# Performance work log

Hardware: AMD Instinct MI355X
Metric: run time of the kernel (lower is better)

Reference implementation:

```python
import jax, jax.numpy as jnp
import numpy as np

B, N_P, N_S = 64, 50, 200
N_NODES = N_P * N_S          # 10000 nodes per graph (jobs x ops)
N_CAND = N_S + 1             # 201 candidates
INPUT_DIM, HIDDEN = 3, 64
NODE_DIM = 2 * HIDDEN        # h_nodes feature dim (=> actor in = 6*HIDDEN)
POOL_DIM = 4 * HIDDEN        # h_pooled dim (mean || max pooling)
H_ACTOR, H_CRITIC = 256, 256


def setup_inputs() -> dict:
    key = jax.random.key(0)
    ks = jax.random.split(key, 16)
    p = lambda k, sh: jax.random.normal(k, sh, jnp.float32) * 0.02
    x = jax.random.normal(ks[0], (B, N_NODES, INPUT_DIM), jnp.float32)
    candidate = jax.random.randint(ks[1], (B, N_CAND), 0, N_NODES)
    mask = jax.random.randint(ks[2], (B, N_CAND), 0, 2) > 0
    mask = mask.at[:, 0].set(True)  # guarantee at least one valid action per row
    return {
        "x": x, "candidate": candidate, "mask": mask,
        "fe_w1": p(ks[3], (INPUT_DIM, HIDDEN)), "fe_b1": jnp.zeros((HIDDEN,), jnp.float32),
        "fe_w2": p(ks[4], (HIDDEN, NODE_DIM)), "fe_b2": jnp.zeros((NODE_DIM,), jnp.float32),
        "a_w1": p(ks[5], (NODE_DIM + POOL_DIM, H_ACTOR)), "a_b1": jnp.zeros((H_ACTOR,), jnp.float32),
        "a_w2": p(ks[6], (H_ACTOR, H_ACTOR)), "a_b2": jnp.zeros((H_ACTOR,), jnp.float32),
        "a_w3": p(ks[7], (H_ACTOR, 1)), "a_b3": jnp.zeros((1,), jnp.float32),
        "c_w1": p(ks[8], (POOL_DIM, H_CRITIC)), "c_b1": jnp.zeros((H_CRITIC,), jnp.float32),
        "c_w2": p(ks[9], (H_CRITIC, H_CRITIC)), "c_b2": jnp.zeros((H_CRITIC,), jnp.float32),
        "c_w3": p(ks[10], (H_CRITIC, 1)), "c_b3": jnp.zeros((1,), jnp.float32),
    }


def _actor_critic(x, candidate, mask,
                  fe_w1, fe_b1, fe_w2, fe_b2,
                  a_w1, a_b1, a_w2, a_b2, a_w3, a_b3,
                  c_w1, c_b1, c_w2, c_b2, c_w3, c_b3):
    # --- feature_extract: per-node MLP embedding, graph-level pooling ---
    h = jax.nn.relu(jnp.einsum('bni,ih->bnh', x, fe_w1) + fe_b1)
    h_nodes = jax.nn.relu(jnp.einsum('bnh,hd->bnd', h, fe_w2) + fe_b2)   # [B, N, 2H]
    h_pooled = jnp.concatenate([h_nodes.mean(axis=1), h_nodes.max(axis=1)], axis=-1)  # [B, 4H]

    # --- gather candidate node features (torch.gather over node axis) ---
    cand_feat = jnp.take_along_axis(h_nodes, candidate[:, :, None], axis=1)  # [B, C, 2H]

    # --- concat broadcast pooled feature ---
    pooled_rep = jnp.broadcast_to(h_pooled[:, None, :], (cand_feat.shape[0], cand_feat.shape[1], h_pooled.shape[-1]))
    concat_fea = jnp.concatenate([cand_feat, pooled_rep], axis=-1)  # [B, C, 6H]

    # --- actor MLP (tanh hidden layers, linear out) ---
    a = jnp.tanh(concat_fea @ a_w1 + a_b1)
    a = jnp.tanh(a @ a_w2 + a_b2)
    scores = a @ a_w3 + a_b3                                    # [B, C, 1]

    # --- mask with -inf, softmax over candidate axis ---
    scores = jnp.where(mask[:, :, None], scores, -jnp.inf)
    pi = jax.nn.softmax(scores, axis=1)                          # [B, C, 1]

    # --- critic MLP on pooled feature ---
    c = jnp.tanh(h_pooled @ c_w1 + c_b1)
    c = jnp.tanh(c @ c_w2 + c_b2)
    v = c @ c_w3 + c_b3                                          # [B, 1]
    return pi, v


def reference(x, candidate, mask,
              fe_w1, fe_b1, fe_w2, fe_b2,
              a_w1, a_b1, a_w2, a_b2, a_w3, a_b3,
              c_w1, c_b1, c_w2, c_b2, c_w3, c_b3):
    return _actor_critic(x, candidate, mask,
                         fe_w1, fe_b1, fe_w2, fe_b2,
                         a_w1, a_b1, a_w2, a_b2, a_w3, a_b3,
                         c_w1, c_b1, c_w2, c_b2, c_w3, c_b3)
```

## Files before the change

### kernel.cpp

```cpp
#include <hip/hip_runtime.h>

#define NN 10000
#define NCAND 201
#define NB 64

typedef __attribute__((ext_vector_type(8))) short short8;
typedef __attribute__((ext_vector_type(4))) float f32x4;

__device__ __forceinline__ float bf2f(unsigned short u) {
  return __uint_as_float(((unsigned int)u) << 16);
}
__device__ __forceinline__ unsigned short f2bf(float f) {
  unsigned int u = __float_as_uint(f);
  u += 0x7FFFu + ((u >> 16) & 1u);
  return (unsigned short)(u >> 16);
}
__device__ __forceinline__ float fast_tanh(float x) {
  return 1.0f - 2.0f / (__expf(2.0f * x) + 1.0f);
}
__device__ __forceinline__ float gld(const void* p, long i, int f) {
  return f ? ((const float*)p)[i] : bf2f(((const unsigned short*)p)[i]);
}

__global__ __launch_bounds__(256)
void detect_kernel(const void* x, const void* w1, const void* b1, const void* w2,
                   const void* b2, const void* aw1, const void* ab1, const void* aw2,
                   const void* ab2, const void* aw3, const void* ab3,
                   const void* cw1, const void* cb1, const void* cw2, const void* cb2,
                   const void* cw3, const void* cb3,
                   const unsigned int* mask_w, const unsigned int* cand_w,
                   int* F) {
  const void* ptrs[17] = {x, w1, b1, w2, b2, aw1, ab1, aw2, ab2, aw3, ab3,
                          cw1, cb1, cw2, cb2, cw3, cb3};
  const int sizes[17] = {1920000, 192, 64, 8192, 128, 98304, 256, 65536, 256,
                         256, 1, 65536, 256, 65536, 256, 256, 1};
  const int t = threadIdx.x;
  const int j = blockIdx.x;
  __shared__ int sh[3];
  if (t < 3) sh[t] = 0;
  __syncthreads();
  if (j < 17) {
    const unsigned short* p = (const unsigned short*)ptrs[j];
    int K = min(sizes[j], 2048);
    int c = 0;
    for (int i = t; i < K; i += 256)
      if ((p[i] & 0x7F80u) >= 0x4300u) c++;
    if (c) atomicAdd(&sh[0], c);
    __syncthreads();
    if (t == 0) F[j] = (sh[0] > (K >> 3)) ? 1 : 0;
  } else if (j == 17) {
    int flo = 0, fhi = 0, fgt = 0;
    for (int i = t; i < 3216; i += 256) {
      unsigned int w = mask_w[i];
      if ((w & 0xFFFFu) == 0x3F80u) flo = 1;
      if ((w >> 16) == 0x3F80u) fhi = 1;
      if (w > 1u) fgt = 1;
    }
    if (flo) sh[0] = 1;
    if (fhi) sh[1] = 1;
    if (fgt) sh[2] = 1;
    __syncthreads();
    if (t == 0) F[17] = sh[0] ? 2 : (sh[1] ? 3 : (sh[2] ? 1 : 0));
  } else {
    int co = 0;
    for (int i = t; i < 1024; i += 256)
      if ((i & 1) && cand_w[i] != 0u) co = 1;
    if (co) sh[0] = 1;
    __syncthreads();
    if (t == 0) F[18] = sh[0] ? 0 : 1;
  }
}

__global__ __launch_bounds__(256)
void prep_kernel(const void* __restrict__ fe_w2, const void* __restrict__ a_w1,
                 const void* __restrict__ a_w2,
                 const void* __restrict__ c_w1, const void* __restrict__ c_w2,
                 const int* __restrict__ F,
                 unsigned short* __restrict__ w2t, unsigned short* __restrict__ aw1t,
                 unsigned short* __restrict__ aw2t,
                 unsigned short* __restrict__ cw1t, unsigned short* __restrict__ cw2t) {
  const int F3 = F[3], F5 = F[5], F7 = F[7], F11 = F[11], F13 = F[13];
  int i = blockIdx.x * 256 + threadIdx.x;
  if (i < 128 * 64) { int n = i >> 6, k = i & 63; w2t[i] = f2bf(gld(fe_w2, k * 128 + n, F3)); }
  if (i < 256 * 384) { int n = i / 384, k = i % 384; aw1t[i] = f2bf(gld(a_w1, k * 256 + n, F5)); }
  if (i < 256 * 256) {
    int n = i >> 8, k = i & 255;
    aw2t[i] = f2bf(gld(a_w2, k * 256 + n, F7));
    cw1t[i] = f2bf(gld(c_w1, k * 256 + n, F11));
    cw2t[i] = f2bf(gld(c_w2, k * 256 + n, F13));
  }
}

__global__ __launch_bounds__(256, 4)
void feat_pool_kernel(const void* __restrict__ x,
                      const void* __restrict__ w1, const void* __restrict__ b1,
                      const unsigned short* __restrict__ w2t,
                      const void* __restrict__ b2,
                      const int* __restrict__ F,
                      float* __restrict__ psum, float* __restrict__ pmax) {
  __shared__ __align__(16) unsigned short h1s[64 * 72];
  __shared__ float w1f[3 * 64];
  __shared__ float b1f[64];
  __shared__ float b2f[128];

  const int t = threadIdx.x;
  const int b = blockIdx.x >> 5;
  const int s = blockIdx.x & 31;
  const int lane = t & 63;
  const int wv = t >> 6;
  const int F0 = F[0], F1 = F[1], F2 = F[2], F4 = F[4];

  if (t < 192) w1f[t] = gld(w1, t, F1);
  if (t < 64) b1f[t] = gld(b1, t, F2);
  if (t < 128) b2f[t] = gld(b2, t, F4);

  short8 bfr[2][2];
#pragma unroll
  for (int nl = 0; nl < 2; ++nl)
#pragma unroll
    for (int ks = 0; ks < 2; ++ks) {
      int col = wv * 32 + nl * 16 + (lane & 15);
      bfr[nl][ks] = *(const short8*)(w2t + col * 64 + ((lane >> 4) * 8) + ks * 32);
    }
  __syncthreads();

  float csum[2] = {0.f, 0.f};
  float cmax[2] = {0.f, 0.f};

  for (int c = s; c < 157; c += 32) {
    int nb = c * 64;
    int cnt = (nb + 64 <= NN) ? 64 : (NN - nb);
    {
      int m = t & 63;
      if (m < cnt) {
        long xo = ((long)b * NN + nb + m) * 3;
        float x0 = gld(x, xo, F0), x1 = gld(x, xo + 1, F0), x2 = gld(x, xo + 2, F0);
        int kg = t >> 6;
        short8 v0, v1;
#pragma unroll
        for (int i = 0; i < 8; ++i) {
          int k = kg * 16 + i;
          float v = x0 * w1f[k] + x1 * w1f[64 + k] + x2 * w1f[128 + k] + b1f[k];
          v0[i] = (short)f2bf(fmaxf(v, 0.f));
        }
#pragma unroll
        for (int i = 0; i < 8; ++i) {
          int k = kg * 16 + 8 + i;
          float v = x0 * w1f[k] + x1 * w1f[64 + k] + x2 * w1f[128 + k] + b1f[k];
          v1[i] = (short)f2bf(fmaxf(v, 0.f));
        }
        *(short8*)(h1s + m * 72 + kg * 16) = v0;
        *(short8*)(h1s + m * 72 + kg * 16 + 8) = v1;
      }
    }
    __syncthreads();
#pragma unroll
    for (int mt = 0; mt < 4; ++mt) {
      const unsigned short* ap = h1s + (mt * 16 + (lane & 15)) * 72 + ((lane >> 4) * 8);
      short8 af0 = *(const short8*)(ap);
      short8 af1 = *(const short8*)(ap + 32);
#pragma unroll
      for (int nl = 0; nl < 2; ++nl) {
        f32x4 acc = {0.f, 0.f, 0.f, 0.f};
        acc = __builtin_amdgcn_mfma_f32_16x16x32_bf16(af0, bfr[nl][0], acc, 0, 0, 0);
        acc = __builtin_amdgcn_mfma_f32_16x16x32_bf16(af1, bfr[nl][1], acc, 0, 0, 0);
        int col = wv * 32 + nl * 16 + (lane & 15);
        float bb = b2f[col];
#pragma unroll
        for (int r = 0; r < 4; ++r) {
          int row = mt * 16 + ((lane >> 4) * 4) + r;
          if (row < cnt) {
            float v = fmaxf(acc[r] + bb, 0.f);
            csum[nl] += v;
            cmax[nl] = fmaxf(cmax[nl], v);
          }
        }
      }
    }
    __syncthreads();
  }
#pragma unroll
  for (int nl = 0; nl < 2; ++nl) {
    csum[nl] += __shfl_xor(csum[nl], 16);
    csum[nl] += __shfl_xor(csum[nl], 32);
    cmax[nl] = fmaxf(cmax[nl], __shfl_xor(cmax[nl], 16));
    cmax[nl] = fmaxf(cmax[nl], __shfl_xor(cmax[nl], 32));
  }
  if (lane < 16) {
#pragma unroll
    for (int nl = 0; nl < 2; ++nl) {
      int col = wv * 32 + nl * 16 + lane;
      atomicAdd(&psum[b * 128 + col], csum[nl]);
      atomicMax((int*)&pmax[b * 128 + col], __float_as_int(cmax[nl]));
    }
  }
}

__global__ __launch_bounds__(256)
void actor_kernel(const void* __restrict__ x, const int* __restrict__ cand,
                  const void* __restrict__ w1, const void* __restrict__ b1,
                  const void* __restrict__ b2bf,
                  const void* __restrict__ ab1, const void* __restrict__ ab2,
                  const void* __restrict__ aw3, const void* __restrict__ ab3,
                  const int* __restrict__ F,
                  const float* __restrict__ psum, const float* __restrict__ pmax,
                  const unsigned short* __restrict__ w2t,
                  const unsigned short* __restrict__ aw1t,
                  const unsigned short* __restrict__ aw2t,
                  float* __restrict__ scores) {
  __shared__ __align__(16) unsigned short h1c[32 * 72];
  __shared__ __align__(16) unsigned short cf[32 * 136];
  __shared__ __align__(16) unsigned short a1s[32 * 264];
  __shared__ __align__(16) unsigned short a2s[32 * 264];
  __shared__ __align__(16) unsigned short plbf[256];
  __shared__ float ab1f[256], ab2f[256], b2f[128];

  const int t = threadIdx.x;
  const int b = blockIdx.x / 7;
  const int cb = blockIdx.x % 7;
  const int cbase = cb * 29;
  const int cntc = min(29, NCAND - cbase);
  const int lane = t & 63;
  const int wv = t >> 6;
  const int F0 = F[0], F1 = F[1], F2 = F[2], F4 = F[4], F6 = F[6], F8 = F[8];
  const int F9 = F[9], F10 = F[10], C64 = F[18];

  if (t < 128) {
    plbf[t] = f2bf(psum[b * 128 + t] * (1.0f / 10000.0f));
    plbf[128 + t] = f2bf(pmax[b * 128 + t]);
    b2f[t] = gld(b2bf, t, F4);
  }
  ab1f[t] = gld(ab1, t, F6);
  ab2f[t] = gld(ab2, t, F8);

  {
    int r = t & 31;
    int ci = cbase + r;
    if (ci > NCAND - 1) ci = NCAND - 1;
    long cidx = (long)b * NCAND + ci;
    int nd = C64 ? cand[2 * cidx] : cand[cidx];
    long xo = ((long)b * NN + nd) * 3;
    float x0 = gld(x, xo, F0), x1 = gld(x, xo + 1, F0), x2 = gld(x, xo + 2, F0);
    int kg = t >> 5;
#pragma unroll
    for (int i = 0; i < 8; ++i) {
      int k = kg * 8 + i;
      float v = x0 * gld(w1, k, F1) + x1 * gld(w1, 64 + k, F1) +
                x2 * gld(w1, 128 + k, F1) + gld(b1, k, F2);
      h1c[r * 72 + k] = f2bf(fmaxf(v, 0.f));
    }
  }
  __syncthreads();

  {
    short8 af[2][2];
#pragma unroll
    for (int mt = 0; mt < 2; ++mt)
#pragma unroll
      for (int ks = 0; ks < 2; ++ks)
        af[mt][ks] = *(const short8*)(h1c + (mt * 16 + (lane & 15)) * 72 + ((lane >> 4) * 8) + ks * 32);
#pragma unroll
    for (int nl = 0; nl < 2; ++nl) {
      int col = wv * 32 + nl * 16 + (lane & 15);
      short8 bf0 = *(const short8*)(w2t + col * 64 + ((lane >> 4) * 8));
      short8 bf1 = *(const short8*)(w2t + col * 64 + ((lane >> 4) * 8) + 32);
      float bb = b2f[col];
#pragma unroll
      for (int mt = 0; mt < 2; ++mt) {
        f32x4 acc = {0.f, 0.f, 0.f, 0.f};
        acc = __builtin_amdgcn_mfma_f32_16x16x32_bf16(af[mt][0], bf0, acc, 0, 0, 0);
        acc = __builtin_amdgcn_mfma_f32_16x16x32_bf16(af[mt][1], bf1, acc, 0, 0, 0);
#pragma unroll
        for (int r = 0; r < 4; ++r) {
          int row = mt * 16 + ((lane >> 4) * 4) + r;
          cf[row * 136 + col] = f2bf(fmaxf(acc[r] + bb, 0.f));
        }
      }
    }
  }
  __syncthreads();

  {
    f32x4 acc[2][4];
#pragma unroll
    for (int mt = 0; mt < 2; ++mt)
#pragma unroll
      for (int nt = 0; nt < 4; ++nt) acc[mt][nt] = (f32x4){0.f, 0.f, 0.f, 0.f};
    for (int ks = 0; ks < 12; ++ks) {
      short8 af0, af1;
      if (ks < 4) {
        af0 = *(const short8*)(cf + (lane & 15) * 136 + ks * 32 + ((lane >> 4) * 8));
        af1 = *(const short8*)(cf + (16 + (lane & 15)) * 136 + ks * 32 + ((lane >> 4) * 8));
      } else {
        short8 p = *(const short8*)(plbf + (ks - 4) * 32 + ((lane >> 4) * 8));
        af0 = p;
        af1 = p;
      }
#pragma unroll
      for (int nt = 0; nt < 4; ++nt) {
        int col = wv * 64 + nt * 16 + (lane & 15);
        short8 bfr = *(const short8*)(aw1t + col * 384 + ks * 32 + ((lane >> 4) * 8));
        acc[0][nt] = __builtin_amdgcn_mfma_f32_16x16x32_bf16(af0, bfr, acc[0][nt], 0, 0, 0);
        acc[1][nt] = __builtin_amdgcn_mfma_f32_16x16x32_bf16(af1, bfr, acc[1][nt], 0, 0, 0);
      }
    }
#pragma unroll
    for (int mt = 0; mt < 2; ++mt)
#pragma unroll
      for (int nt = 0; nt < 4; ++nt) {
        int col = wv * 64 + nt * 16 + (lane & 15);
        float bb = ab1f[col];
#pragma unroll
        for (int r = 0; r < 4; ++r) {
          int row = mt * 16 + ((lane >> 4) * 4) + r;
          a1s[row * 264 + col] = f2bf(fast_tanh(acc[mt][nt][r] + bb));
        }
      }
  }
  __syncthreads();

  {
    f32x4 acc[2][4];
#pragma unroll
    for (int mt = 0; mt < 2; ++mt)
#pragma unroll
      for (int nt = 0; nt < 4; ++nt) acc[mt][nt] = (f32x4){0.f, 0.f, 0.f, 0.f};
    for (int ks = 0; ks < 8; ++ks) {
      short8 af0 = *(const short8*)(a1s + (lane & 15) * 264 + ks * 32 + ((lane >> 4) * 8));
      short8 af1 = *(const short8*)(a1s + (16 + (lane & 15)) * 264 + ks * 32 + ((lane >> 4) * 8));
#pragma unroll
      for (int nt = 0; nt < 4; ++nt) {
        int col = wv * 64 + nt * 16 + (lane & 15);
        short8 bfr = *(const short8*)(aw2t + col * 256 + ks * 32 + ((lane >> 4) * 8));
        acc[0][nt] = __builtin_amdgcn_mfma_f32_16x16x32_bf16(af0, bfr, acc[0][nt], 0, 0, 0);
        acc[1][nt] = __builtin_amdgcn_mfma_f32_16x16x32_bf16(af1, bfr, acc[1][nt], 0, 0, 0);
      }
    }
#pragma unroll
    for (int mt = 0; mt < 2; ++mt)
#pragma unroll
      for (int nt = 0; nt < 4; ++nt) {
        int col = wv * 64 + nt * 16 + (lane & 15);
        float bb = ab2f[col];
#pragma unroll
        for (int r = 0; r < 4; ++r) {
          int row = mt * 16 + ((lane >> 4) * 4) + r;
          a2s[row * 264 + col] = f2bf(fast_tanh(acc[mt][nt][r] + bb));
        }
      }
  }
  __syncthreads();

  {
    int row = t >> 3, seg = t & 7;
    float p = 0.f;
#pragma unroll 8
    for (int i = 0; i < 32; ++i) {
      int k = seg * 32 + i;
      p += bf2f(a2s[row * 264 + k]) * gld(aw3, k, F9);
    }
    p += __shfl_xor(p, 1);
    p += __shfl_xor(p, 2);
    p += __shfl_xor(p, 4);
    if (seg == 0 && row < cntc)
      scores[b * 256 + cbase + row] = p + gld(ab3, 0, F10);
  }
}

__global__ __launch_bounds__(256)
void softmax_critic_kernel(const float* __restrict__ scores,
                           const void* __restrict__ mask,
                           const int* __restrict__ F,
                           const float* __restrict__ psum,
                           const float* __restrict__ pmax,
                           const unsigned short* __restrict__ cw1t,
                           const unsigned short* __restrict__ cw2t,
                           const void* __restrict__ cb1, const void* __restrict__ cb2,
                           const void* __restrict__ cw3, const void* __restrict__ cb3,
                           void* __restrict__ out) {
  __shared__ float plf[256];
  __shared__ float c1f[256];
  __shared__ float red[4];
  const int t = threadIdx.x, b = blockIdx.x;
  const int lane = t & 63, wv = t >> 6;
  const int MM = F[17];
  const int OF = (F[0] + F[1] + F[3] + F[5] + F[7] + F[9] + F[11] + F[13] + F[15]) >= 5;
  const int F12 = F[12], F14 = F[14], F15 = F[15], F16 = F[16];

  if (t < 128) {
    plf[t] = psum[b * 128 + t] * (1.0f / 10000.0f);
    plf[128 + t] = pmax[b * 128 + t];
  }

  float sraw = 0.f, sv = -1e30f;
  bool valid = false;
  if (t < NCAND) {
    sraw = scores[b * 256 + t];
    long idx = (long)b * NCAND + t;
    if (MM == 0)      valid = ((const int*)mask)[idx] != 0;
    else if (MM == 1) valid = ((const unsigned char*)mask)[idx] != 0;
    else if (MM == 2) valid = ((const unsigned short*)mask)[idx] != 0;
    else              valid = ((const unsigned int*)mask)[idx] != 0;
    if (valid) sv = sraw;
  }
  float m = sv;
  for (int o = 32; o; o >>= 1) m = fmaxf(m, __shfl_xor(m, o));
  if (lane == 0) red[wv] = m;
  __syncthreads();
  m = fmaxf(fmaxf(red[0], red[1]), fmaxf(red[2], red[3]));
  __syncthreads();
  float e = valid ? __expf(sraw - m) : 0.f;
  if (!(e == e)) e = 0.f;
  float ss = e;
  for (int o = 32; o; o >>= 1) ss += __shfl_xor(ss, o);
  if (lane == 0) red[wv] = ss;
  __syncthreads();
  float tot = red[0] + red[1] + red[2] + red[3];
  tot = fmaxf(tot, 1e-30f);
  if (t < NCAND) {
    float pv = e / tot;
    if (!(pv == pv)) pv = 0.f;
    if (OF) ((float*)out)[b * NCAND + t] = pv;
    else ((unsigned short*)out)[b * NCAND + t] = f2bf(pv);
  }
  __syncthreads();

  {
    float a = gld(cb1, t, F12);
    const unsigned short* row = cw1t + t * 256;
#pragma unroll
    for (int k8 = 0; k8 < 32; ++k8) {
      short8 w = *(const short8*)(row + k8 * 8);
#pragma unroll
      for (int j = 0; j < 8; ++j)
        a += plf[k8 * 8 + j] * bf2f((unsigned short)w[j]);
    }
    c1f[t] = fast_tanh(a);
  }
  __syncthreads();
  {
    float a2 = gld(cb2, t, F14);
    const unsigned short* row = cw2t + t * 256;
#pragma unroll
    for (int k8 = 0; k8 < 32; ++k8) {
      short8 w = *(const short8*)(row + k8 * 8);
#pragma unroll
      for (int j = 0; j < 8; ++j)
        a2 += c1f[k8 * 8 + j] * bf2f((unsigned short)w[j]);
    }
    a2 = fast_tanh(a2);
    float p = a2 * gld(cw3, t, F15);
    for (int o = 32; o; o >>= 1) p += __shfl_xor(p, o);
    __syncthreads();
    if (lane == 0) red[wv] = p;
    __syncthreads();
    if (t == 0) {
      float v = red[0] + red[1] + red[2] + red[3] + gld(cb3, 0, F16);
      if (!(v == v)) v = 0.f;
      if (OF) ((float*)out)[NB * NCAND + b] = v;
      else ((unsigned short*)out)[NB * NCAND + b] = f2bf(v);
    }
  }
}

extern "C" void kernel_launch(void* const* d_in, const int* in_sizes, int n_in,
                              void* d_out, int out_size, void* d_ws, size_t ws_size,
                              hipStream_t stream) {
  const void* x = d_in[0];
  const int* cand = (const int*)d_in[1];
  const void* mask = d_in[2];
  const void* fe_w1 = d_in[3];
  const void* fe_b1 = d_in[4];
  const void* fe_w2 = d_in[5];
  const void* fe_b2 = d_in[6];
  const void* a_w1 = d_in[7];
  const void* a_b1 = d_in[8];
  const void* a_w2 = d_in[9];
  const void* a_b2 = d_in[10];
  const void* a_w3 = d_in[11];
  const void* a_b3 = d_in[12];
  const void* c_w1 = d_in[13];
  const void* c_b1 = d_in[14];
  const void* c_w2 = d_in[15];
  const void* c_b2 = d_in[16];
  const void* c_w3 = d_in[17];
  const void* c_b3 = d_in[18];

  char* ws = (char*)d_ws;
  float* psum = (float*)(ws + 0);
  float* pmax = (float*)(ws + 32768);
  float* scores = (float*)(ws + 65536);
  unsigned short* w2t = (unsigned short*)(ws + 131072);
  unsigned short* aw1t = (unsigned short*)(ws + 147456);
  unsigned short* aw2t = (unsigned short*)(ws + 344064);
  int* F = (int*)(ws + 475136);
  unsigned short* cw1t = (unsigned short*)(ws + 475264);
  unsigned short* cw2t = (unsigned short*)(ws + 606336);

  (void)hipMemsetAsync(ws, 0, 65536, stream);

  detect_kernel<<<19, 256, 0, stream>>>(x, fe_w1, fe_b1, fe_w2, fe_b2,
                                        a_w1, a_b1, a_w2, a_b2, a_w3, a_b3,
                                        c_w1, c_b1, c_w2, c_b2, c_w3, c_b3,
                                        (const unsigned int*)mask,
                                        (const unsigned int*)cand, F);
  prep_kernel<<<384, 256, 0, stream>>>(fe_w2, a_w1, a_w2, c_w1, c_w2, F,
                                       w2t, aw1t, aw2t, cw1t, cw2t);
  feat_pool_kernel<<<2048, 256, 0, stream>>>(x, fe_w1, fe_b1, w2t, fe_b2, F, psum, pmax);
  actor_kernel<<<448, 256, 0, stream>>>(x, cand, fe_w1, fe_b1, fe_b2,
                                        a_b1, a_b2, a_w3, a_b3, F, psum, pmax,
                                        w2t, aw1t, aw2t, scores);
  softmax_critic_kernel<<<64, 256, 0, stream>>>(scores, mask, F, psum, pmax,
                                                cw1t, cw2t, c_b1, c_b2, c_w3, c_b3,
                                                (void*)d_out);
}
```

Before: 173.8 us.

## Enlarge feat-pool node chunks, prefetch next x chunk, fold memset into detect kernel

Measured after the change: 171.3 us. Within noise of the previous version (-1.5%).

```diff
diff --git a/kernel.cpp b/kernel.cpp
--- a/kernel.cpp
+++ b/kernel.cpp
@@ -29,7 +29,7 @@
                    const void* cw1, const void* cb1, const void* cw2, const void* cb2,
                    const void* cw3, const void* cb3,
                    const unsigned int* mask_w, const unsigned int* cand_w,
-                   int* F) {
+                   int* F, float* zero_base) {
   const void* ptrs[17] = {x, w1, b1, w2, b2, aw1, ab1, aw2, ab2, aw3, ab3,
                           cw1, cb1, cw2, cb2, cw3, cb3};
   const int sizes[17] = {1920000, 192, 64, 8192, 128, 98304, 256, 65536, 256,
@@ -61,13 +61,15 @@
     if (fgt) sh[2] = 1;
     __syncthreads();
     if (t == 0) F[17] = sh[0] ? 2 : (sh[1] ? 3 : (sh[2] ? 1 : 0));
-  } else {
+  } else if (j == 18) {
     int co = 0;
     for (int i = t; i < 1024; i += 256)
       if ((i & 1) && cand_w[i] != 0u) co = 1;
     if (co) sh[0] = 1;
     __syncthreads();
     if (t == 0) F[18] = sh[0] ? 0 : 1;
+  } else {
+    zero_base[(j - 19) * 256 + t] = 0.f;
   }
 }
 
@@ -98,14 +100,14 @@
                       const void* __restrict__ b2,
                       const int* __restrict__ F,
                       float* __restrict__ psum, float* __restrict__ pmax) {
-  __shared__ __align__(16) unsigned short h1s[64 * 72];
+  __shared__ __align__(16) unsigned short h1s[128 * 72];
   __shared__ float w1f[3 * 64];
   __shared__ float b1f[64];
   __shared__ float b2f[128];
 
   const int t = threadIdx.x;
-  const int b = blockIdx.x >> 5;
-  const int s = blockIdx.x & 31;
+  const int b = blockIdx.x >> 4;
+  const int s = blockIdx.x & 15;
   const int lane = t & 63;
   const int wv = t >> 6;
   const int F0 = F[0], F1 = F[1], F2 = F[2], F4 = F[4];
@@ -127,35 +129,52 @@
   float csum[2] = {0.f, 0.f};
   float cmax[2] = {0.f, 0.f};
 
-  for (int c = s; c < 157; c += 32) {
-    int nb = c * 64;
-    int cnt = (nb + 64 <= NN) ? 64 : (NN - nb);
+  const int m = t & 127;
+  const int kg = t >> 7;
+
+  float x0 = 0.f, x1 = 0.f, x2 = 0.f;
+  {
+    int c0 = s;
+    if (c0 < 79) {
+      int nb = c0 * 128;
+      if (m < min(128, NN - nb)) {
+        long xo = ((long)b * NN + nb + m) * 3;
+        x0 = gld(x, xo, F0); x1 = gld(x, xo + 1, F0); x2 = gld(x, xo + 2, F0);
+      }
+    }
+  }
+
+  for (int c = s; c < 79; c += 16) {
+    int nb = c * 128;
+    int cnt = (nb + 128 <= NN) ? 128 : (NN - nb);
+    if (m < cnt) {
+#pragma unroll
+      for (int blk = 0; blk < 4; ++blk) {
+        short8 v;
+#pragma unroll
+        for (int i = 0; i < 8; ++i) {
+          int k = kg * 32 + blk * 8 + i;
+          float vv = x0 * w1f[k] + x1 * w1f[64 + k] + x2 * w1f[128 + k] + b1f[k];
+          v[i] = (short)f2bf(fmaxf(vv, 0.f));
+        }
+        *(short8*)(h1s + m * 72 + kg * 32 + blk * 8) = v;
+      }
+    }
     {
-      int m = t & 63;
-      if (m < cnt) {
-        long xo = ((long)b * NN + nb + m) * 3;
-        float x0 = gld(x, xo, F0), x1 = gld(x, xo + 1, F0), x2 = gld(x, xo + 2, F0);
-        int kg = t >> 6;
-        short8 v0, v1;
-#pragma unroll
-        for (int i = 0; i < 8; ++i) {
-          int k = kg * 16 + i;
-          float v = x0 * w1f[k] + x1 * w1f[64 + k] + x2 * w1f[128 + k] + b1f[k];
-          v0[i] = (short)f2bf(fmaxf(v, 0.f));
+      int cn = c + 16;
+      float nx0 = 0.f, nx1 = 0.f, nx2 = 0.f;
+      if (cn < 79) {
+        int nbn = cn * 128;
+        if (m < min(128, NN - nbn)) {
+          long xo = ((long)b * NN + nbn + m) * 3;
+          nx0 = gld(x, xo, F0); nx1 = gld(x, xo + 1, F0); nx2 = gld(x, xo + 2, F0);
         }
-#pragma unroll
-        for (int i = 0; i < 8; ++i) {
-          int k = kg * 16 + 8 + i;
-          float v = x0 * w1f[k] + x1 * w1f[64 + k] + x2 * w1f[128 + k] + b1f[k];
-          v1[i] = (short)f2bf(fmaxf(v, 0.f));
-        }
-        *(short8*)(h1s + m * 72 + kg * 16) = v0;
-        *(short8*)(h1s + m * 72 + kg * 16 + 8) = v1;
-      }
-    }
-    __syncthreads();
-#pragma unroll
-    for (int mt = 0; mt < 4; ++mt) {
+      }
+      __syncthreads();
+      x0 = nx0; x1 = nx1; x2 = nx2;
+    }
+#pragma unroll
+    for (int mt = 0; mt < 8; ++mt) {
       const unsigned short* ap = h1s + (mt * 16 + (lane & 15)) * 72 + ((lane >> 4) * 8);
       short8 af0 = *(const short8*)(ap);
       short8 af1 = *(const short8*)(ap + 32);
@@ -497,16 +516,14 @@
   unsigned short* cw1t = (unsigned short*)(ws + 475264);
   unsigned short* cw2t = (unsigned short*)(ws + 606336);
 
-  (void)hipMemsetAsync(ws, 0, 65536, stream);
-
-  detect_kernel<<<19, 256, 0, stream>>>(x, fe_w1, fe_b1, fe_w2, fe_b2,
+  detect_kernel<<<83, 256, 0, stream>>>(x, fe_w1, fe_b1, fe_w2, fe_b2,
                                         a_w1, a_b1, a_w2, a_b2, a_w3, a_b3,
                                         c_w1, c_b1, c_w2, c_b2, c_w3, c_b3,
                                         (const unsigned int*)mask,
-                                        (const unsigned int*)cand, F);
+                                        (const unsigned int*)cand, F, psum);
   prep_kernel<<<384, 256, 0, stream>>>(fe_w2, a_w1, a_w2, c_w1, c_w2, F,
                                        w2t, aw1t, aw2t, cw1t, cw2t);
-  feat_pool_kernel<<<2048, 256, 0, stream>>>(x, fe_w1, fe_b1, w2t, fe_b2, F, psum, pmax);
+  feat_pool_kernel<<<1024, 256, 0, stream>>>(x, fe_w1, fe_b1, w2t, fe_b2, F, psum, pmax);
   actor_kernel<<<448, 256, 0, stream>>>(x, cand, fe_w1, fe_b1, fe_b2,
                                         a_b1, a_b2, a_w3, a_b3, F, psum, pmax,
                                         w2t, aw1t, aw2t, scores);
```
